# Kernel optimization log

Measured on AMD Instinct MI355X. Metric: run time of the kernel, lower is better.

Reference implementation:

```python
import jax, jax.numpy as jnp
import numpy as np

HIDDEN = 768
HEADS = 12
HEAD_DIM = HIDDEN // HEADS
BETA = 0.5
BANDWIDTH = 1.0
D_INTRINSIC = 3
LN_EPS = 1e-12


def setup_inputs() -> dict:
    key = jax.random.key(0)
    ks = jax.random.split(key, 10)
    B, S, E = 2, 2048, HIDDEN
    sc = 1.0 / np.sqrt(E)
    return {
        "hidden_states": jax.random.normal(ks[0], (B, S, E), jnp.float32),
        "attention_mask": jnp.zeros((B, S), jnp.float32),
        "Wq": jax.random.normal(ks[1], (E, E), jnp.float32) * sc,
        "bq": jax.random.normal(ks[2], (E,), jnp.float32) * 0.02,
        "Wv": jax.random.normal(ks[3], (E, E), jnp.float32) * sc,
        "bv": jax.random.normal(ks[4], (E,), jnp.float32) * 0.02,
        "Wo": jax.random.normal(ks[5], (E, E), jnp.float32) * sc,
        "bo": jax.random.normal(ks[6], (E,), jnp.float32) * 0.02,
        "ln_g": jnp.ones((E,), jnp.float32),
        "ln_b": jnp.zeros((E,), jnp.float32),
    }


def _layernorm(x, g, b, eps=LN_EPS):
    mu = jnp.mean(x, axis=-1, keepdims=True)
    var = jnp.mean((x - mu) ** 2, axis=-1, keepdims=True)
    return (x - mu) * jax.lax.rsqrt(var + eps) * g + b


def reference(hidden_states, attention_mask, Wq, bq, Wv, bv, Wo, bo, ln_g, ln_b):
    B, S, E = hidden_states.shape
    H, D = HEADS, HEAD_DIM
    # projections (torch Linear: x @ W.T + b)
    q = (hidden_states @ Wq.T + bq).reshape(B, S, H, D).transpose(0, 2, 1, 3)  # [B,H,S,D]
    v = (hidden_states @ Wv.T + bv).reshape(B, S, H, D).transpose(0, 2, 1, 3)  # [B,H,S,D]
    # pairwise Euclidean distance (cdist) via norm expansion, safe sqrt
    qn = jnp.sum(q * q, axis=-1)  # [B,H,S]
    d2 = qn[:, :, :, None] + qn[:, :, None, :] - 2.0 * jnp.einsum("bhid,bhjd->bhij", q, q)
    dist = jnp.sqrt(jnp.maximum(d2, 1e-12))  # [B,H,S,S]
    # mask: positions with attention_mask < 0 get distance 2
    keep = (attention_mask >= 0)  # [B,S]
    pair_keep = keep[:, None, :, None] & keep[:, None, None, :]  # [B,1,S,S]
    dist = jnp.where(pair_keep, dist, 2.0)
    # power-law score + softmax
    attn_score = (1.0 + dist / (BANDWIDTH ** 0.5)) ** (-D_INTRINSIC - BETA)
    attn = jax.nn.softmax(attn_score, axis=-1)
    out = jnp.einsum("bhij,bhjd->bhid", attn, v)  # [B,H,S,D]
    out = out.transpose(0, 2, 1, 3).reshape(B, S, E)
    # ModelSelfOutput: dense + residual + LayerNorm (dropout=0, eval)
    out = out @ Wo.T + bo
    return _layernorm(out + hidden_states, ln_g, ln_b)
```

## Files before the change

kernel.cpp:

```cpp
#include <hip/hip_runtime.h>
#include <hip/hip_bf16.h>
#include <cstdint>
#include <cstddef>

#define S_LEN 2048
#define NH 12
#define HD 64
#define EDIM 768

typedef short bf16x8 __attribute__((ext_vector_type(8)));
typedef float f32x4  __attribute__((ext_vector_type(4)));

__device__ __forceinline__ unsigned short f2bf(float f) {
    return __bfloat16_as_ushort(__float2bfloat16(f));
}
__device__ __forceinline__ float bf2f(unsigned short u) {
    union { unsigned int i; float f; } x;
    x.i = ((unsigned int)u) << 16;
    return x.f;
}
__device__ __forceinline__ float rsq_f32(float x) {
#if __has_builtin(__builtin_amdgcn_rsqf)
    return __builtin_amdgcn_rsqf(x);
#else
    return __builtin_amdgcn_rcpf(__builtin_amdgcn_sqrtf(x));
#endif
}

__global__ __launch_bounds__(256) void precast_kernel(
    const float* __restrict__ hs, const float* __restrict__ Wq,
    const float* __restrict__ Wv, const float* __restrict__ Wo,
    unsigned short* __restrict__ hsb, unsigned short* __restrict__ Wqvb,
    unsigned short* __restrict__ Wob)
{
    const int i4 = blockIdx.x * 256 + threadIdx.x;
    const float* src;
    unsigned short* dst;
    int rel;
    if (i4 < 786432)        { src = hs; dst = hsb;            rel = i4; }
    else if (i4 < 933888)   { src = Wq; dst = Wqvb;           rel = i4 - 786432; }
    else if (i4 < 1081344)  { src = Wv; dst = Wqvb + 589824;  rel = i4 - 933888; }
    else                    { src = Wo; dst = Wob;            rel = i4 - 1081344; }
    float4 v = ((const float4*)src)[rel];
    ushort4 o;
    o.x = f2bf(v.x); o.y = f2bf(v.y); o.z = f2bf(v.z); o.w = f2bf(v.w);
    ((ushort4*)dst)[rel] = o;
}

__global__ __launch_bounds__(256) void qv_gemm(
    const unsigned short* __restrict__ hsb, const unsigned short* __restrict__ Wqvb,
    const float* __restrict__ bq, const float* __restrict__ bv,
    unsigned short* __restrict__ Qb, unsigned short* __restrict__ Vt,
    float* __restrict__ qn)
{
    __shared__ __align__(16) unsigned short As[64][40];
    __shared__ __align__(16) unsigned short Bs[128][40];

    const int t  = threadIdx.x;
    const int m0 = blockIdx.y << 6;
    const int c0 = blockIdx.x << 7;
    const bool isQ = (c0 < EDIM);
    const float* bias = isQ ? bq : bv;
    const int cb = isQ ? c0 : (c0 - EDIM);

    const int w  = t >> 6;
    const int l  = t & 63;
    const int ll = l & 15;
    const int lq = l >> 4;
    const int wx = w & 1;
    const int wy = w >> 1;

    const int srowA = t & 63;
    const int skA   = (t >> 6) << 3;
    const int srowB = t & 127;
    const int skB   = (t >> 7) << 4;

    f32x4 acc[2][4];
#pragma unroll
    for (int m = 0; m < 2; m++)
#pragma unroll
        for (int n = 0; n < 4; n++) acc[m][n] = (f32x4){0.f, 0.f, 0.f, 0.f};

    for (int k0 = 0; k0 < EDIM; k0 += 32) {
        bf16x8 va  = *(const bf16x8*)(hsb  + (size_t)(m0 + srowA) * EDIM + k0 + skA);
        bf16x8 vb0 = *(const bf16x8*)(Wqvb + (size_t)(c0 + srowB) * EDIM + k0 + skB);
        bf16x8 vb1 = *(const bf16x8*)(Wqvb + (size_t)(c0 + srowB) * EDIM + k0 + skB + 8);
        __syncthreads();
        *(bf16x8*)&As[srowA][skA]     = va;
        *(bf16x8*)&Bs[srowB][skB]     = vb0;
        *(bf16x8*)&Bs[srowB][skB + 8] = vb1;
        __syncthreads();
        bf16x8 aF[2], bF[4];
#pragma unroll
        for (int m = 0; m < 2; m++)
            aF[m] = *(const bf16x8*)&As[(wy << 5) + (m << 4) + ll][lq << 3];
#pragma unroll
        for (int n = 0; n < 4; n++)
            bF[n] = *(const bf16x8*)&Bs[(wx << 6) + (n << 4) + ll][lq << 3];
#pragma unroll
        for (int m = 0; m < 2; m++)
#pragma unroll
            for (int n = 0; n < 4; n++)
                acc[m][n] = __builtin_amdgcn_mfma_f32_16x16x32_bf16(aF[m], bF[n], acc[m][n], 0, 0, 0);
    }

    const int hcol0 = cb + (wx << 6);
    const int h = hcol0 >> 6;
    const int rowbase = m0 + (wy << 5);
    const int b = rowbase >> 11;
    const int sbase = rowbase & 2047;

    if (isQ) {
#pragma unroll
        for (int m = 0; m < 2; m++) {
#pragma unroll
            for (int r = 0; r < 4; r++) {
                const int si = sbase + (m << 4) + (lq << 2) + r;
                unsigned short* qrow = Qb + ((size_t)(b * NH + h) * S_LEN + si) * HD;
                float qsq = 0.f;
#pragma unroll
                for (int n = 0; n < 4; n++) {
                    unsigned short u = f2bf(acc[m][n][r] + bias[hcol0 + (n << 4) + ll]);
                    qrow[(n << 4) + ll] = u;
                    float f = bf2f(u);
                    qsq += f * f;
                }
                qsq += __shfl_xor(qsq, 1);
                qsq += __shfl_xor(qsq, 2);
                qsq += __shfl_xor(qsq, 4);
                qsq += __shfl_xor(qsq, 8);
                if (ll == 0) qn[(b * NH + h) * S_LEN + si] = qsq;
            }
        }
    } else {
#pragma unroll
        for (int m = 0; m < 2; m++) {
            const int si = sbase + (m << 4) + (lq << 2);
#pragma unroll
            for (int n = 0; n < 4; n++) {
                ushort4 o;
                o.x = f2bf(acc[m][n][0] + bias[hcol0 + (n << 4) + ll]);
                o.y = f2bf(acc[m][n][1] + bias[hcol0 + (n << 4) + ll]);
                o.z = f2bf(acc[m][n][2] + bias[hcol0 + (n << 4) + ll]);
                o.w = f2bf(acc[m][n][3] + bias[hcol0 + (n << 4) + ll]);
                *(ushort4*)&Vt[((size_t)(b * NH + h) * HD + (n << 4) + ll) * S_LEN + si] = o;
            }
        }
    }
}

template<int CUR>
__device__ __forceinline__ void attn_tile(
    int j0, int jn,
    const unsigned short* __restrict__ Qbase,
    const unsigned short* __restrict__ Vbase,
    const float* __restrict__ qnb, const float* __restrict__ mb,
    int ll, int lq,
    const bf16x8 (&aQ)[2][2],
    const float (&qni)[2][4], const float (&keepi)[2][4],
    const bf16x8& ones,
    f32x4 (&oacc)[2][4], f32x4 (&wacc)[2],
    bf16x8 (&nb0)[2], bf16x8 (&nb1)[2],
    bf16x8 (&vbuf)[2][4],
    unsigned short (&Wt)[2][2][16][40])
{
    constexpr int PRV = CUR ^ 1;
    __builtin_amdgcn_wave_barrier();
#pragma unroll
    for (int m = 0; m < 4; m++)
        vbuf[CUR][m] = *(const bf16x8*)(Vbase + (size_t)((m << 4) + ll) * S_LEN + j0 + (lq << 3));
    float qnjv[2], kjf[2];
#pragma unroll
    for (int n = 0; n < 2; n++) {
        int jc = j0 + (n << 4) + ll;
        qnjv[n] = qnb[jc];
        kjf[n]  = (mb[jc] >= 0.f) ? 1.f : 0.f;
    }
    f32x4 s[2][2];
#pragma unroll
    for (int s2 = 0; s2 < 2; s2++)
#pragma unroll
        for (int n = 0; n < 2; n++) {
            f32x4 c = (f32x4){0.f, 0.f, 0.f, 0.f};
            c = __builtin_amdgcn_mfma_f32_16x16x32_bf16(aQ[s2][0], nb0[n], c, 0, 0, 0);
            c = __builtin_amdgcn_mfma_f32_16x16x32_bf16(aQ[s2][1], nb1[n], c, 0, 0, 0);
            s[s2][n] = c;
        }
#pragma unroll
    for (int n = 0; n < 2; n++) {
        const unsigned short* bp = Qbase + (size_t)(jn + (n << 4) + ll) * HD + (lq << 3);
        nb0[n] = *(const bf16x8*)bp;
        nb1[n] = *(const bf16x8*)(bp + 32);
    }
#pragma unroll
    for (int s2 = 0; s2 < 2; s2++) {
        bf16x8 aP = *(const bf16x8*)&Wt[PRV][s2][ll][lq << 3];
#pragma unroll
        for (int m = 0; m < 4; m++)
            oacc[s2][m] = __builtin_amdgcn_mfma_f32_16x16x32_bf16(aP, vbuf[PRV][m], oacc[s2][m], 0, 0, 0);
        wacc[s2] = __builtin_amdgcn_mfma_f32_16x16x32_bf16(aP, ones, wacc[s2], 0, 0, 0);
    }
#pragma unroll
    for (int s2 = 0; s2 < 2; s2++)
#pragma unroll
        for (int n = 0; n < 2; n++)
#pragma unroll
            for (int r = 0; r < 4; r++) {
                float d2   = fmaf(-2.f, s[s2][n][r], qni[s2][r] + qnjv[n]);
                float dist = __builtin_amdgcn_sqrtf(fmaxf(d2, 1e-12f));
                dist = (keepi[s2][r] * kjf[n] != 0.f) ? dist : 2.0f;
                float x  = 1.0f + dist;
                float x2 = x * x;
                float x7 = x2 * x2 * x2 * x;
                float p  = rsq_f32(x7);
                float wv = fmaf(fmaf(fmaf(fmaf(0.041666668f, p, 0.16666667f),
                                          p, 0.5f), p, 1.0f), p, 1.0f);
                union { float f; unsigned int u; } cv; cv.f = wv;
                Wt[CUR][s2][(lq << 2) + r][(n << 4) + ll] =
                    (unsigned short)((cv.u + 0x8000u) >> 16);
            }
}

__global__ __launch_bounds__(64) void attn_kernel(
    const unsigned short* __restrict__ Qb, const unsigned short* __restrict__ Vt,
    const float* __restrict__ qn, const float* __restrict__ mask,
    unsigned short* __restrict__ AObf)
{
    __shared__ __align__(16) unsigned short Wt[2][2][16][40];

    const int l  = threadIdx.x;
    const int ll = l & 15;
    const int lq = l >> 4;
    const int id = blockIdx.x;
    const int ib = id / 24;
    const int bh = id - ib * 24;
    const int b  = bh / NH;
    const int h  = bh - b * NH;
    const int iw = ib << 5;

    const unsigned short* Qbase = Qb + ((size_t)bh << 17);
    const unsigned short* Vbase = Vt + ((size_t)bh << 17);
    const float* qnb = qn + (bh << 11);
    const float* mb  = mask + (b << 11);

    bf16x8 aQ[2][2];
#pragma unroll
    for (int s2 = 0; s2 < 2; s2++) {
        const unsigned short* qp = Qbase + (size_t)(iw + (s2 << 4) + ll) * HD + (lq << 3);
        aQ[s2][0] = *(const bf16x8*)qp;
        aQ[s2][1] = *(const bf16x8*)(qp + 32);
    }

    float qni[2][4], keepi[2][4];
#pragma unroll
    for (int s2 = 0; s2 < 2; s2++)
#pragma unroll
        for (int r = 0; r < 4; r++) {
            int row = iw + (s2 << 4) + (lq << 2) + r;
            qni[s2][r]   = qnb[row];
            keepi[s2][r] = (mb[row] >= 0.f) ? 1.f : 0.f;
        }

    bf16x8 ones;
#pragma unroll
    for (int i = 0; i < 8; i++) ones[i] = (short)0x3F80;

    f32x4 oacc[2][4];
#pragma unroll
    for (int s2 = 0; s2 < 2; s2++)
#pragma unroll
        for (int m = 0; m < 4; m++) oacc[s2][m] = (f32x4){0.f, 0.f, 0.f, 0.f};
    f32x4 wacc[2];
    wacc[0] = (f32x4){0.f, 0.f, 0.f, 0.f};
    wacc[1] = (f32x4){0.f, 0.f, 0.f, 0.f};

    bf16x8 nb0[2], nb1[2];
#pragma unroll
    for (int n = 0; n < 2; n++) {
        const unsigned short* bp = Qbase + (size_t)((n << 4) + ll) * HD + (lq << 3);
        nb0[n] = *(const bf16x8*)bp;
        nb1[n] = *(const bf16x8*)(bp + 32);
    }
    bf16x8 vbuf[2][4];

    {
#pragma unroll
        for (int m = 0; m < 4; m++)
            vbuf[0][m] = *(const bf16x8*)(Vbase + (size_t)((m << 4) + ll) * S_LEN + (lq << 3));
        float qnjv[2], kjf[2];
#pragma unroll
        for (int n = 0; n < 2; n++) {
            int jc = (n << 4) + ll;
            qnjv[n] = qnb[jc];
            kjf[n]  = (mb[jc] >= 0.f) ? 1.f : 0.f;
        }
        f32x4 s[2][2];
#pragma unroll
        for (int s2 = 0; s2 < 2; s2++)
#pragma unroll
            for (int n = 0; n < 2; n++) {
                f32x4 c = (f32x4){0.f, 0.f, 0.f, 0.f};
                c = __builtin_amdgcn_mfma_f32_16x16x32_bf16(aQ[s2][0], nb0[n], c, 0, 0, 0);
                c = __builtin_amdgcn_mfma_f32_16x16x32_bf16(aQ[s2][1], nb1[n], c, 0, 0, 0);
                s[s2][n] = c;
            }
#pragma unroll
        for (int n = 0; n < 2; n++) {
            const unsigned short* bp = Qbase + (size_t)(32 + (n << 4) + ll) * HD + (lq << 3);
            nb0[n] = *(const bf16x8*)bp;
            nb1[n] = *(const bf16x8*)(bp + 32);
        }
#pragma unroll
        for (int s2 = 0; s2 < 2; s2++)
#pragma unroll
            for (int n = 0; n < 2; n++)
#pragma unroll
                for (int r = 0; r < 4; r++) {
                    float d2   = fmaf(-2.f, s[s2][n][r], qni[s2][r] + qnjv[n]);
                    float dist = __builtin_amdgcn_sqrtf(fmaxf(d2, 1e-12f));
                    dist = (keepi[s2][r] * kjf[n] != 0.f) ? dist : 2.0f;
                    float x  = 1.0f + dist;
                    float x2 = x * x;
                    float x7 = x2 * x2 * x2 * x;
                    float p  = rsq_f32(x7);
                    float wv = fmaf(fmaf(fmaf(fmaf(0.041666668f, p, 0.16666667f),
                                              p, 0.5f), p, 1.0f), p, 1.0f);
                    union { float f; unsigned int u; } cv; cv.f = wv;
                    Wt[0][s2][(lq << 2) + r][(n << 4) + ll] =
                        (unsigned short)((cv.u + 0x8000u) >> 16);
                }
    }

    for (int base = 1; base <= 61; base += 2) {
        attn_tile<1>(base << 5, (base + 1) << 5, Qbase, Vbase, qnb, mb, ll, lq,
                     aQ, qni, keepi, ones, oacc, wacc, nb0, nb1, vbuf, Wt);
        attn_tile<0>((base + 1) << 5, (base + 2) << 5, Qbase, Vbase, qnb, mb, ll, lq,
                     aQ, qni, keepi, ones, oacc, wacc, nb0, nb1, vbuf, Wt);
    }
    attn_tile<1>(63 << 5, 0, Qbase, Vbase, qnb, mb, ll, lq,
                 aQ, qni, keepi, ones, oacc, wacc, nb0, nb1, vbuf, Wt);

    __builtin_amdgcn_wave_barrier();
#pragma unroll
    for (int s2 = 0; s2 < 2; s2++) {
        bf16x8 aP = *(const bf16x8*)&Wt[1][s2][ll][lq << 3];
#pragma unroll
        for (int m = 0; m < 4; m++)
            oacc[s2][m] = __builtin_amdgcn_mfma_f32_16x16x32_bf16(aP, vbuf[1][m], oacc[s2][m], 0, 0, 0);
        wacc[s2] = __builtin_amdgcn_mfma_f32_16x16x32_bf16(aP, ones, wacc[s2], 0, 0, 0);
    }

#pragma unroll
    for (int s2 = 0; s2 < 2; s2++)
#pragma unroll
        for (int r = 0; r < 4; r++) {
            float inv = 1.0f / wacc[s2][r];
            const int row = iw + (s2 << 4) + (lq << 2) + r;
            unsigned short* dst = AObf + (size_t)((b << 11) + row) * EDIM + (h << 6);
#pragma unroll
            for (int m = 0; m < 4; m++)
                dst[(m << 4) + ll] = f2bf(oacc[s2][m][r] * inv);
        }
}

__global__ __launch_bounds__(256) void oproj_gemm(
    const unsigned short* __restrict__ AObf, const unsigned short* __restrict__ Wob,
    const float* __restrict__ bo, const float* __restrict__ hs,
    float* __restrict__ TMP)
{
    __shared__ __align__(16) unsigned short As[64][40];
    __shared__ __align__(16) unsigned short Bs[64][40];

    const int t  = threadIdx.x;
    const int m0 = blockIdx.y << 6;
    const int c0 = blockIdx.x << 6;

    const int w  = t >> 6;
    const int l  = t & 63;
    const int ll = l & 15;
    const int lq = l >> 4;
    const int wx = w & 1;
    const int wy = w >> 1;

    const int srow = t & 63;
    const int sk   = (t >> 6) << 3;

    f32x4 acc[2][2];
#pragma unroll
    for (int m = 0; m < 2; m++)
#pragma unroll
        for (int n = 0; n < 2; n++) acc[m][n] = (f32x4){0.f, 0.f, 0.f, 0.f};

    for (int k0 = 0; k0 < EDIM; k0 += 32) {
        bf16x8 va = *(const bf16x8*)(AObf + (size_t)(m0 + srow) * EDIM + k0 + sk);
        bf16x8 vb = *(const bf16x8*)(Wob  + (size_t)(c0 + srow) * EDIM + k0 + sk);
        __syncthreads();
        *(bf16x8*)&As[srow][sk] = va;
        *(bf16x8*)&Bs[srow][sk] = vb;
        __syncthreads();
        bf16x8 aF[2], bF[2];
#pragma unroll
        for (int m = 0; m < 2; m++)
            aF[m] = *(const bf16x8*)&As[(wy << 5) + (m << 4) + ll][lq << 3];
#pragma unroll
        for (int n = 0; n < 2; n++)
            bF[n] = *(const bf16x8*)&Bs[(wx << 5) + (n << 4) + ll][lq << 3];
#pragma unroll
        for (int m = 0; m < 2; m++)
#pragma unroll
            for (int n = 0; n < 2; n++)
                acc[m][n] = __builtin_amdgcn_mfma_f32_16x16x32_bf16(aF[m], bF[n], acc[m][n], 0, 0, 0);
    }

#pragma unroll
    for (int m = 0; m < 2; m++) {
#pragma unroll
        for (int r = 0; r < 4; r++) {
            const int row = m0 + (wy << 5) + (m << 4) + (lq << 2) + r;
#pragma unroll
            for (int n = 0; n < 2; n++) {
                const int col = c0 + (wx << 5) + (n << 4) + ll;
                TMP[(size_t)row * EDIM + col] =
                    acc[m][n][r] + bo[col] + hs[(size_t)row * EDIM + col];
            }
        }
    }
}

__global__ __launch_bounds__(256) void ln_kernel(
    const float* __restrict__ X, const float* __restrict__ g,
    const float* __restrict__ be, float* __restrict__ out)
{
    const int row = blockIdx.x;
    const int t = threadIdx.x;
    const float* x = X + (size_t)row * EDIM;

    float s = 0.f, sq = 0.f;
#pragma unroll
    for (int c = t; c < EDIM; c += 256) {
        float v = x[c];
        s += v; sq += v * v;
    }
#pragma unroll
    for (int m = 1; m < 64; m <<= 1) {
        s  += __shfl_xor(s, m);
        sq += __shfl_xor(sq, m);
    }
    __shared__ float ss[4], ssq[4];
    const int w = t >> 6;
    if ((t & 63) == 0) { ss[w] = s; ssq[w] = sq; }
    __syncthreads();
    s  = ss[0] + ss[1] + ss[2] + ss[3];
    sq = ssq[0] + ssq[1] + ssq[2] + ssq[3];
    const float mu  = s * (1.f / EDIM);
    const float var = sq * (1.f / EDIM) - mu * mu;
    const float rstd = 1.0f / sqrtf(var + 1e-12f);

#pragma unroll
    for (int c = t; c < EDIM; c += 256) {
        out[(size_t)row * EDIM + c] = (x[c] - mu) * rstd * g[c] + be[c];
    }
}

extern "C" void kernel_launch(void* const* d_in, const int* in_sizes, int n_in,
                              void* d_out, int out_size, void* d_ws, size_t ws_size,
                              hipStream_t stream) {
    const float* hs   = (const float*)d_in[0];
    const float* mask = (const float*)d_in[1];
    const float* Wq   = (const float*)d_in[2];
    const float* bq   = (const float*)d_in[3];
    const float* Wv   = (const float*)d_in[4];
    const float* bv   = (const float*)d_in[5];
    const float* Wo   = (const float*)d_in[6];
    const float* bo   = (const float*)d_in[7];
    const float* g    = (const float*)d_in[8];
    const float* be   = (const float*)d_in[9];

    char* w8 = (char*)d_ws;
    unsigned short* Qb   = (unsigned short*)(w8);
    unsigned short* Vt   = (unsigned short*)(w8 +  6291456);
    float*          qn   = (float*)        (w8 + 12582912);
    unsigned short* AObf = (unsigned short*)(w8 + 12779520);
    unsigned short* hsb  = (unsigned short*)(w8 + 19070976);
    unsigned short* Wqvb = (unsigned short*)(w8 + 25362432);
    unsigned short* Wob  = (unsigned short*)(w8 + 27721728);
    float*          TMP  = (float*)(w8);

    precast_kernel<<<dim3(4800),    256, 0, stream>>>(hs, Wq, Wv, Wo, hsb, Wqvb, Wob);
    qv_gemm       <<<dim3(12, 64),  256, 0, stream>>>(hsb, Wqvb, bq, bv, Qb, Vt, qn);
    attn_kernel   <<<dim3(1536),    64,  0, stream>>>(Qb, Vt, qn, mask, AObf);
    oproj_gemm    <<<dim3(12, 64),  256, 0, stream>>>(AObf, Wob, bo, hs, TMP);
    ln_kernel     <<<dim3(4096),    256, 0, stream>>>(TMP, g, be, (float*)d_out);
}
```

Measured before the change: 261.3 us.

## Split attention key range across two waves with LDS reduction

The attention kernel now runs two wavefronts per block. Each wave processes half of the 2048 keys for the same 32 query rows, and the partial output and weight-sum accumulators are then combined through shared memory before normalization and store. This doubles the wave count (1536 blocks of 64 threads was 1536 waves on 256 CUs) to improve latency hiding and occupancy. The cost is extra LDS, a block barrier, a reduction step, and duplicated per-wave Q loads.

```diff
diff --git a/kernel.cpp b/kernel.cpp
--- a/kernel.cpp
+++ b/kernel.cpp
@@ -221,14 +221,17 @@
             }
 }
 
-__global__ __launch_bounds__(64) void attn_kernel(
+__global__ __launch_bounds__(128) void attn_kernel(
     const unsigned short* __restrict__ Qb, const unsigned short* __restrict__ Vt,
     const float* __restrict__ qn, const float* __restrict__ mask,
     unsigned short* __restrict__ AObf)
 {
-    __shared__ __align__(16) unsigned short Wt[2][2][16][40];
-
-    const int l  = threadIdx.x;
+    __shared__ __align__(16) unsigned short Wts[2][2][2][16][40];
+    __shared__ __align__(16) float Red[64][40];
+
+    const int t  = threadIdx.x;
+    const int w  = t >> 6;
+    const int l  = t & 63;
     const int ll = l & 15;
     const int lq = l >> 4;
     const int id = blockIdx.x;
@@ -237,6 +240,7 @@
     const int b  = bh / NH;
     const int h  = bh - b * NH;
     const int iw = ib << 5;
+    const int jbase = w << 10;
 
     const unsigned short* Qbase = Qb + ((size_t)bh << 17);
     const unsigned short* Vbase = Vt + ((size_t)bh << 17);
@@ -277,7 +281,7 @@
     bf16x8 nb0[2], nb1[2];
 #pragma unroll
     for (int n = 0; n < 2; n++) {
-        const unsigned short* bp = Qbase + (size_t)((n << 4) + ll) * HD + (lq << 3);
+        const unsigned short* bp = Qbase + (size_t)(jbase + (n << 4) + ll) * HD + (lq << 3);
         nb0[n] = *(const bf16x8*)bp;
         nb1[n] = *(const bf16x8*)(bp + 32);
     }
@@ -286,11 +290,11 @@
     {
 #pragma unroll
         for (int m = 0; m < 4; m++)
-            vbuf[0][m] = *(const bf16x8*)(Vbase + (size_t)((m << 4) + ll) * S_LEN + (lq << 3));
+            vbuf[0][m] = *(const bf16x8*)(Vbase + (size_t)((m << 4) + ll) * S_LEN + jbase + (lq << 3));
         float qnjv[2], kjf[2];
 #pragma unroll
         for (int n = 0; n < 2; n++) {
-            int jc = (n << 4) + ll;
+            int jc = jbase + (n << 4) + ll;
             qnjv[n] = qnb[jc];
             kjf[n]  = (mb[jc] >= 0.f) ? 1.f : 0.f;
         }
@@ -306,7 +310,7 @@
             }
 #pragma unroll
         for (int n = 0; n < 2; n++) {
-            const unsigned short* bp = Qbase + (size_t)(32 + (n << 4) + ll) * HD + (lq << 3);
+            const unsigned short* bp = Qbase + (size_t)(jbase + 32 + (n << 4) + ll) * HD + (lq << 3);
             nb0[n] = *(const bf16x8*)bp;
             nb1[n] = *(const bf16x8*)(bp + 32);
         }
@@ -326,41 +330,64 @@
                     float wv = fmaf(fmaf(fmaf(fmaf(0.041666668f, p, 0.16666667f),
                                               p, 0.5f), p, 1.0f), p, 1.0f);
                     union { float f; unsigned int u; } cv; cv.f = wv;
-                    Wt[0][s2][(lq << 2) + r][(n << 4) + ll] =
+                    Wts[w][0][s2][(lq << 2) + r][(n << 4) + ll] =
                         (unsigned short)((cv.u + 0x8000u) >> 16);
                 }
     }
 
-    for (int base = 1; base <= 61; base += 2) {
-        attn_tile<1>(base << 5, (base + 1) << 5, Qbase, Vbase, qnb, mb, ll, lq,
-                     aQ, qni, keepi, ones, oacc, wacc, nb0, nb1, vbuf, Wt);
-        attn_tile<0>((base + 1) << 5, (base + 2) << 5, Qbase, Vbase, qnb, mb, ll, lq,
-                     aQ, qni, keepi, ones, oacc, wacc, nb0, nb1, vbuf, Wt);
-    }
-    attn_tile<1>(63 << 5, 0, Qbase, Vbase, qnb, mb, ll, lq,
-                 aQ, qni, keepi, ones, oacc, wacc, nb0, nb1, vbuf, Wt);
+    for (int base = 1; base <= 29; base += 2) {
+        attn_tile<1>(jbase + (base << 5), jbase + ((base + 1) << 5),
+                     Qbase, Vbase, qnb, mb, ll, lq,
+                     aQ, qni, keepi, ones, oacc, wacc, nb0, nb1, vbuf, Wts[w]);
+        attn_tile<0>(jbase + ((base + 1) << 5), jbase + ((base + 2) << 5),
+                     Qbase, Vbase, qnb, mb, ll, lq,
+                     aQ, qni, keepi, ones, oacc, wacc, nb0, nb1, vbuf, Wts[w]);
+    }
+    attn_tile<1>(jbase + (31 << 5), jbase,
+                 Qbase, Vbase, qnb, mb, ll, lq,
+                 aQ, qni, keepi, ones, oacc, wacc, nb0, nb1, vbuf, Wts[w]);
 
     __builtin_amdgcn_wave_barrier();
 #pragma unroll
     for (int s2 = 0; s2 < 2; s2++) {
-        bf16x8 aP = *(const bf16x8*)&Wt[1][s2][ll][lq << 3];
+        bf16x8 aP = *(const bf16x8*)&Wts[w][1][s2][ll][lq << 3];
 #pragma unroll
         for (int m = 0; m < 4; m++)
             oacc[s2][m] = __builtin_amdgcn_mfma_f32_16x16x32_bf16(aP, vbuf[1][m], oacc[s2][m], 0, 0, 0);
         wacc[s2] = __builtin_amdgcn_mfma_f32_16x16x32_bf16(aP, ones, wacc[s2], 0, 0, 0);
     }
 
-#pragma unroll
-    for (int s2 = 0; s2 < 2; s2++)
-#pragma unroll
-        for (int r = 0; r < 4; r++) {
-            float inv = 1.0f / wacc[s2][r];
-            const int row = iw + (s2 << 4) + (lq << 2) + r;
-            unsigned short* dst = AObf + (size_t)((b << 11) + row) * EDIM + (h << 6);
+    if (w == 1) {
+#pragma unroll
+        for (int s2 = 0; s2 < 2; s2++)
 #pragma unroll
             for (int m = 0; m < 4; m++)
-                dst[(m << 4) + ll] = f2bf(oacc[s2][m][r] * inv);
-        }
+                *(f32x4*)&Red[l][(s2 << 4) + (m << 2)] = oacc[s2][m];
+        *(f32x4*)&Red[l][32] = wacc[0];
+        *(f32x4*)&Red[l][36] = wacc[1];
+    }
+    __syncthreads();
+    if (w == 0) {
+#pragma unroll
+        for (int s2 = 0; s2 < 2; s2++)
+#pragma unroll
+            for (int m = 0; m < 4; m++)
+                oacc[s2][m] += *(const f32x4*)&Red[l][(s2 << 4) + (m << 2)];
+        wacc[0] += *(const f32x4*)&Red[l][32];
+        wacc[1] += *(const f32x4*)&Red[l][36];
+
+#pragma unroll
+        for (int s2 = 0; s2 < 2; s2++)
+#pragma unroll
+            for (int r = 0; r < 4; r++) {
+                float inv = 1.0f / wacc[s2][r];
+                const int row = iw + (s2 << 4) + (lq << 2) + r;
+                unsigned short* dst = AObf + (size_t)((b << 11) + row) * EDIM + (h << 6);
+#pragma unroll
+                for (int m = 0; m < 4; m++)
+                    dst[(m << 4) + ll] = f2bf(oacc[s2][m][r] * inv);
+            }
+    }
 }
 
 __global__ __launch_bounds__(256) void oproj_gemm(
@@ -488,7 +515,7 @@
 
     precast_kernel<<<dim3(4800),    256, 0, stream>>>(hs, Wq, Wv, Wo, hsb, Wqvb, Wob);
     qv_gemm       <<<dim3(12, 64),  256, 0, stream>>>(hsb, Wqvb, bq, bv, Qb, Vt, qn);
-    attn_kernel   <<<dim3(1536),    64,  0, stream>>>(Qb, Vt, qn, mask, AObf);
+    attn_kernel   <<<dim3(1536),    128, 0, stream>>>(Qb, Vt, qn, mask, AObf);
     oproj_gemm    <<<dim3(12, 64),  256, 0, stream>>>(AObf, Wob, bo, hs, TMP);
     ln_kernel     <<<dim3(4096),    256, 0, stream>>>(TMP, g, be, (float*)d_out);
 }
```

Measured after the change: 272.1 us. 4.1% more time.

## Split attention key dimension in two and add reduction kernel

Applied to the files above, without the earlier changes.

The attention kernel now splits the 2048 keys into two halves, doubling the grid to 3072 single-wave blocks. Each block writes unnormalized fp32 partial outputs and weight sums, and a new reduce kernel adds the halves, normalizes and writes bf16. The aim is better occupancy and latency hiding on a GPU with many CUs, since 1536 one-wave blocks underfill it. The cost is an extra launch plus roughly 25 MB of fp32 partial writes and reads.

```diff
diff --git a/kernel.cpp b/kernel.cpp
--- a/kernel.cpp
+++ b/kernel.cpp
@@ -224,7 +224,7 @@
 __global__ __launch_bounds__(64) void attn_kernel(
     const unsigned short* __restrict__ Qb, const unsigned short* __restrict__ Vt,
     const float* __restrict__ qn, const float* __restrict__ mask,
-    unsigned short* __restrict__ AObf)
+    float* __restrict__ Pacc, float* __restrict__ Wsum)
 {
     __shared__ __align__(16) unsigned short Wt[2][2][16][40];
 
@@ -232,11 +232,13 @@
     const int ll = l & 15;
     const int lq = l >> 4;
     const int id = blockIdx.x;
-    const int ib = id / 24;
-    const int bh = id - ib * 24;
+    const int outer = id / 24;
+    const int bh = id - outer * 24;
+    const int ib = outer >> 1;
+    const int jh = outer & 1;
     const int b  = bh / NH;
-    const int h  = bh - b * NH;
     const int iw = ib << 5;
+    const int jbase = jh << 10;
 
     const unsigned short* Qbase = Qb + ((size_t)bh << 17);
     const unsigned short* Vbase = Vt + ((size_t)bh << 17);
@@ -277,7 +279,7 @@
     bf16x8 nb0[2], nb1[2];
 #pragma unroll
     for (int n = 0; n < 2; n++) {
-        const unsigned short* bp = Qbase + (size_t)((n << 4) + ll) * HD + (lq << 3);
+        const unsigned short* bp = Qbase + (size_t)(jbase + (n << 4) + ll) * HD + (lq << 3);
         nb0[n] = *(const bf16x8*)bp;
         nb1[n] = *(const bf16x8*)(bp + 32);
     }
@@ -286,11 +288,11 @@
     {
 #pragma unroll
         for (int m = 0; m < 4; m++)
-            vbuf[0][m] = *(const bf16x8*)(Vbase + (size_t)((m << 4) + ll) * S_LEN + (lq << 3));
+            vbuf[0][m] = *(const bf16x8*)(Vbase + (size_t)((m << 4) + ll) * S_LEN + jbase + (lq << 3));
         float qnjv[2], kjf[2];
 #pragma unroll
         for (int n = 0; n < 2; n++) {
-            int jc = (n << 4) + ll;
+            int jc = jbase + (n << 4) + ll;
             qnjv[n] = qnb[jc];
             kjf[n]  = (mb[jc] >= 0.f) ? 1.f : 0.f;
         }
@@ -306,7 +308,7 @@
             }
 #pragma unroll
         for (int n = 0; n < 2; n++) {
-            const unsigned short* bp = Qbase + (size_t)(32 + (n << 4) + ll) * HD + (lq << 3);
+            const unsigned short* bp = Qbase + (size_t)(jbase + 32 + (n << 4) + ll) * HD + (lq << 3);
             nb0[n] = *(const bf16x8*)bp;
             nb1[n] = *(const bf16x8*)(bp + 32);
         }
@@ -331,13 +333,16 @@
                 }
     }
 
-    for (int base = 1; base <= 61; base += 2) {
-        attn_tile<1>(base << 5, (base + 1) << 5, Qbase, Vbase, qnb, mb, ll, lq,
+    for (int base = 1; base <= 29; base += 2) {
+        attn_tile<1>(jbase + (base << 5), jbase + ((base + 1) << 5),
+                     Qbase, Vbase, qnb, mb, ll, lq,
                      aQ, qni, keepi, ones, oacc, wacc, nb0, nb1, vbuf, Wt);
-        attn_tile<0>((base + 1) << 5, (base + 2) << 5, Qbase, Vbase, qnb, mb, ll, lq,
+        attn_tile<0>(jbase + ((base + 1) << 5), jbase + ((base + 2) << 5),
+                     Qbase, Vbase, qnb, mb, ll, lq,
                      aQ, qni, keepi, ones, oacc, wacc, nb0, nb1, vbuf, Wt);
     }
-    attn_tile<1>(63 << 5, 0, Qbase, Vbase, qnb, mb, ll, lq,
+    attn_tile<1>(jbase + (31 << 5), jbase,
+                 Qbase, Vbase, qnb, mb, ll, lq,
                  aQ, qni, keepi, ones, oacc, wacc, nb0, nb1, vbuf, Wt);
 
     __builtin_amdgcn_wave_barrier();
@@ -350,17 +355,47 @@
         wacc[s2] = __builtin_amdgcn_mfma_f32_16x16x32_bf16(aP, ones, wacc[s2], 0, 0, 0);
     }
 
+    float* pbase = Pacc + (((size_t)jh * 24 + bh) << 17);
+    float* wbase = Wsum + (((size_t)jh * 24 + bh) << 11);
 #pragma unroll
     for (int s2 = 0; s2 < 2; s2++)
 #pragma unroll
         for (int r = 0; r < 4; r++) {
-            float inv = 1.0f / wacc[s2][r];
             const int row = iw + (s2 << 4) + (lq << 2) + r;
-            unsigned short* dst = AObf + (size_t)((b << 11) + row) * EDIM + (h << 6);
+            float* dst = pbase + ((size_t)row << 6);
 #pragma unroll
             for (int m = 0; m < 4; m++)
-                dst[(m << 4) + ll] = f2bf(oacc[s2][m][r] * inv);
-        }
+                dst[(m << 4) + ll] = oacc[s2][m][r];
+            if (ll == 0) wbase[row] = wacc[s2][r];
+        }
+}
+
+__global__ __launch_bounds__(256) void attn_reduce_kernel(
+    const float* __restrict__ Pacc, const float* __restrict__ Wsum,
+    unsigned short* __restrict__ AObf)
+{
+    const int id = blockIdx.x;
+    const int k  = id / 24;
+    const int bh = id - k * 24;
+    const int b  = bh / NH;
+    const int h  = bh - b * NH;
+    const int t  = threadIdx.x;
+    const int r  = t >> 4;
+    const int d0 = (t & 15) << 2;
+    const int i  = (k << 4) + r;
+
+    const size_t off0 = ((((size_t)0 * 24 + bh) << 11) + i);
+    const size_t off1 = ((((size_t)1 * 24 + bh) << 11) + i);
+    f32x4 o0 = *(const f32x4*)(Pacc + (off0 << 6) + d0);
+    f32x4 o1 = *(const f32x4*)(Pacc + (off1 << 6) + d0);
+    float wsum = Wsum[off0] + Wsum[off1];
+    float inv = 1.0f / wsum;
+    ushort4 o;
+    o.x = f2bf((o0[0] + o1[0]) * inv);
+    o.y = f2bf((o0[1] + o1[1]) * inv);
+    o.z = f2bf((o0[2] + o1[2]) * inv);
+    o.w = f2bf((o0[3] + o1[3]) * inv);
+    *(ushort4*)(AObf + ((size_t)((b << 11) + i)) * EDIM + (h << 6) + d0) = o;
 }
 
 __global__ __launch_bounds__(256) void oproj_gemm(
@@ -484,11 +519,14 @@
     unsigned short* hsb  = (unsigned short*)(w8 + 19070976);
     unsigned short* Wqvb = (unsigned short*)(w8 + 25362432);
     unsigned short* Wob  = (unsigned short*)(w8 + 27721728);
+    float*          Pacc = (float*)        (w8 + 28901376);
+    float*          Wsum = (float*)        (w8 + 54067200);
     float*          TMP  = (float*)(w8);
 
-    precast_kernel<<<dim3(4800),    256, 0, stream>>>(hs, Wq, Wv, Wo, hsb, Wqvb, Wob);
-    qv_gemm       <<<dim3(12, 64),  256, 0, stream>>>(hsb, Wqvb, bq, bv, Qb, Vt, qn);
-    attn_kernel   <<<dim3(1536),    64,  0, stream>>>(Qb, Vt, qn, mask, AObf);
-    oproj_gemm    <<<dim3(12, 64),  256, 0, stream>>>(AObf, Wob, bo, hs, TMP);
-    ln_kernel     <<<dim3(4096),    256, 0, stream>>>(TMP, g, be, (float*)d_out);
-}
+    precast_kernel    <<<dim3(4800),    256, 0, stream>>>(hs, Wq, Wv, Wo, hsb, Wqvb, Wob);
+    qv_gemm           <<<dim3(12, 64),  256, 0, stream>>>(hsb, Wqvb, bq, bv, Qb, Vt, qn);
+    attn_kernel       <<<dim3(3072),    64,  0, stream>>>(Qb, Vt, qn, mask, Pacc, Wsum);
+    attn_reduce_kernel<<<dim3(3072),    256, 0, stream>>>(Pacc, Wsum, AObf);
+    oproj_gemm        <<<dim3(12, 64),  256, 0, stream>>>(AObf, Wob, bo, hs, TMP);
+    ln_kernel         <<<dim3(4096),    256, 0, stream>>>(TMP, g, be, (float*)d_out);
+}
```

After: 272.5 us. +4.3%, slower.
